# Kernel optimization log

Hardware: AMD Instinct MI355X
Metric: run time of the kernel (lower is better)

## Reference

```python
import jax, jax.numpy as jnp
import numpy as np

NEG_SLOPE = 0.1
BN_EPS = 1e-5

def leaky(x):
    return jnp.where(x >= 0, x, NEG_SLOPE * x)

def batchnorm(x, gamma, beta):
    # BatchNorm1d in training mode: biased batch stats over rows
    mu = jnp.mean(x, axis=0)
    var = jnp.var(x, axis=0)
    return gamma * (x - mu) * jax.lax.rsqrt(var + BN_EPS) + beta

def scatter_mean(x, idx, num_segments):
    s = jax.ops.segment_sum(x, idx, num_segments=num_segments)
    c = jax.ops.segment_sum(jnp.ones((x.shape[0], 1), x.dtype), idx, num_segments=num_segments)
    return s / jnp.maximum(c, 1.0)

def setup_inputs() -> dict:
    key = jax.random.key(0)
    ks = jax.random.split(key, 24)
    N, NF, MD, MO = 100000, 400000, 25000, 25000
    Cin, Cout = 64, 128
    Ch = Cout // 2
    def lin(k, fi, fo):
        kw, kb = jax.random.split(k)
        bound = 1.0 / np.sqrt(fi)
        W = jax.random.uniform(kw, (fi, fo), jnp.float32, -bound, bound)
        b = jax.random.uniform(kb, (fo,), jnp.float32, -bound, bound)
        return W, b
    W_in, b_in = lin(ks[0], Cin, Cout)
    W1, b1 = lin(ks[1], Cin, Ch)
    W2, b2 = lin(ks[2], Ch, Ch)
    W3, b3 = lin(ks[3], Ch, Cout)
    W4, b4 = lin(ks[4], 2 * Cout, Cout)
    W5, b5 = lin(ks[5], Cout, Cout)
    return {
        'features': jax.random.normal(ks[6], (N, Cin), jnp.float32),
        'inv': jax.random.randint(ks[7], (N,), 0, MD),
        'coors_inv_cur': jax.random.randint(ks[8], (NF,), 0, N),
        'coors_inv_next': jax.random.randint(ks[9], (NF,), 0, MO),
        'n_down': MD, 'n_out': MO,
        'W_in': W_in, 'b_in': b_in,
        'W1': W1, 'b1': b1, 'g1': jnp.ones((Ch,)), 'be1': jnp.zeros((Ch,)),
        'W2': W2, 'b2': b2, 'g2': jnp.ones((Ch,)), 'be2': jnp.zeros((Ch,)),
        'W3': W3, 'b3': b3,
        'W4': W4, 'b4': b4, 'W5': W5, 'b5': b5,
    }

def reference(features, inv, coors_inv_cur, coors_inv_next, n_down, n_out,
              W_in, b_in, W1, b1, g1, be1, W2, b2, g2, be2, W3, b3,
              W4, b4, W5, b5):
    # downsample: voxel-mean pooling of current-scale features  [MD, Cin]
    down = scatter_mean(features, inv, n_down)
    # identity branch  [N, Cout]
    identity = leaky(features @ W_in + b_in)
    # PPmodel MLP on pooled voxels
    h = batchnorm(leaky(down @ W1 + b1), g1, be1)
    h = batchnorm(leaky(h @ W2 + b2), g2, be2)
    h = leaky(h @ W3 + b3)                      # [MD, Cout]
    out = jnp.concatenate([identity, h[inv]], axis=1)   # [N, 2*Cout]
    g = out[coors_inv_cur]                      # gather to full points [NF, 2*Cout]
    g = leaky(g @ W4 + b4) @ W5 + b5            # layer_out [NF, Cout]
    v_feat = scatter_mean(g, coors_inv_next, n_out)      # [MO, Cout]
    return v_feat
```

## Files before the change

### kernel.cpp

```cpp
#include <hip/hip_runtime.h>
#include <hip/hip_bf16.h>

#define NEG_SLOPE 0.1f
#define BN_EPS 1e-5f
#define MDV 25000
#define CAPI 64
#define CAPD 32

typedef __bf16 bf16_t;
typedef bf16_t bf16x8 __attribute__((ext_vector_type(8)));
typedef float f32x4 __attribute__((ext_vector_type(4)));

__device__ __forceinline__ float leaky(float x) { return x >= 0.0f ? x : NEG_SLOPE * x; }

__global__ void k_setup(int4* __restrict__ zp, int n4, int nz,
                        const float* __restrict__ W4, const float* __restrict__ W5,
                        const float* __restrict__ Win, const float* __restrict__ W1,
                        bf16_t* __restrict__ P1, bf16_t* __restrict__ P2,
                        bf16_t* __restrict__ P0, bf16_t* __restrict__ P4) {
    if ((int)blockIdx.x < nz) {
        int i = blockIdx.x * 256 + threadIdx.x;
        if (i < n4) zp[i] = make_int4(0, 0, 0, 0);
        return;
    }
    int tid = (blockIdx.x - nz) * 256 + threadIdx.x;
    if (tid < 7168) {
        const float* W; bf16_t* P; int t;
        if (tid < 4096)      { W = W4;  P = P1; t = tid; }
        else if (tid < 6144) { W = W5;  P = P2; t = tid - 4096; }
        else                 { W = Win; P = P0; t = tid - 6144; }
        int l = t & 63;
        int sn = t >> 6;
        int col = (sn & 7) * 16 + (l & 15);
        int k0 = (sn >> 3) * 32 + (l >> 4) * 8;
        bf16_t* dst = P + (size_t)t * 8;
#pragma unroll
        for (int j = 0; j < 8; j++) dst[j] = (bf16_t)W[(size_t)(k0 + j) * 128 + col];
    } else if (tid < 7680) {
        int t = tid - 7168;
        int l = t & 63;
        int sn = t >> 6;
        int col = (sn & 3) * 16 + (l & 15);
        int k0 = (sn >> 2) * 32 + (l >> 4) * 8;
        bf16_t* dst = P4 + (size_t)t * 8;
#pragma unroll
        for (int j = 0; j < 8; j++) dst[j] = (bf16_t)W1[(size_t)(k0 + j) * 64 + col];
    }
}

__device__ __forceinline__ void two_gemm_tile(
        const float* __restrict__ in, const bf16_t* __restrict__ Pa,
        const float* __restrict__ ba, const bf16_t* __restrict__ Pb,
        const float* __restrict__ bb, bf16_t* __restrict__ out,
        int M, int base, bf16_t* A, bf16_t* C) {
    int tid = threadIdx.x;
    int valid = M - base; if (valid > 64) valid = 64;

    {
        int r = tid >> 2, q = tid & 3;
        float4 v[4];
        if (r < valid) {
            const float4* src = reinterpret_cast<const float4*>(in + (size_t)(base + r) * 64 + q * 16);
#pragma unroll
            for (int i = 0; i < 4; i++) v[i] = src[i];
        } else {
#pragma unroll
            for (int i = 0; i < 4; i++) v[i] = make_float4(0.f, 0.f, 0.f, 0.f);
        }
        bf16x8 h0, h1;
#pragma unroll
        for (int i = 0; i < 2; i++) {
            h0[i * 4 + 0] = (bf16_t)v[i].x; h0[i * 4 + 1] = (bf16_t)v[i].y;
            h0[i * 4 + 2] = (bf16_t)v[i].z; h0[i * 4 + 3] = (bf16_t)v[i].w;
            h1[i * 4 + 0] = (bf16_t)v[2 + i].x; h1[i * 4 + 1] = (bf16_t)v[2 + i].y;
            h1[i * 4 + 2] = (bf16_t)v[2 + i].z; h1[i * 4 + 3] = (bf16_t)v[2 + i].w;
        }
        int xa = (r & 7) << 3;
        *reinterpret_cast<bf16x8*>(&A[r * 64 + ((q * 16) ^ xa)]) = h0;
        *reinterpret_cast<bf16x8*>(&A[r * 64 + ((q * 16 + 8) ^ xa)]) = h1;
    }
    __syncthreads();

    int w = tid >> 6, l = tid & 63;
    int lg = l >> 4, lr = l & 15;
    int xr = (lr & 7) << 3;

    f32x4 acc[4][2];
#pragma unroll
    for (int t = 0; t < 2; t++) {
        float bv = ba[w * 32 + t * 16 + lr];
#pragma unroll
        for (int m = 0; m < 4; m++) acc[m][t] = (f32x4){bv, bv, bv, bv};
    }
#pragma unroll
    for (int s = 0; s < 2; s++) {
        bf16x8 a[4];
#pragma unroll
        for (int m = 0; m < 4; m++)
            a[m] = *reinterpret_cast<const bf16x8*>(&A[(m * 16 + lr) * 64 + (((s * 4 + lg) * 8) ^ xr)]);
#pragma unroll
        for (int t = 0; t < 2; t++) {
            bf16x8 b = *reinterpret_cast<const bf16x8*>(Pa + ((size_t)(s * 8 + w * 2 + t) * 64 + l) * 8);
#pragma unroll
            for (int m = 0; m < 4; m++)
                acc[m][t] = __builtin_amdgcn_mfma_f32_16x16x32_bf16(a[m], b, acc[m][t], 0, 0, 0);
        }
    }
#pragma unroll
    for (int m = 0; m < 4; m++)
#pragma unroll
        for (int t = 0; t < 2; t++)
#pragma unroll
            for (int rr = 0; rr < 4; rr++) {
                int row = m * 16 + lg * 4 + rr;
                int col = w * 32 + t * 16 + lr;
                C[row * 128 + (col ^ ((row & 7) << 3))] = (bf16_t)leaky(acc[m][t][rr]);
            }
    __syncthreads();

    f32x4 acc2[4][2];
#pragma unroll
    for (int t = 0; t < 2; t++) {
        float bv = bb ? bb[w * 32 + t * 16 + lr] : 0.0f;
#pragma unroll
        for (int m = 0; m < 4; m++) acc2[m][t] = (f32x4){bv, bv, bv, bv};
    }
#pragma unroll
    for (int s = 0; s < 4; s++) {
        bf16x8 a[4];
#pragma unroll
        for (int m = 0; m < 4; m++)
            a[m] = *reinterpret_cast<const bf16x8*>(&C[(m * 16 + lr) * 128 + ((s * 32 + lg * 8) ^ xr)]);
#pragma unroll
        for (int t = 0; t < 2; t++) {
            bf16x8 b = *reinterpret_cast<const bf16x8*>(Pb + ((size_t)(s * 8 + w * 2 + t) * 64 + l) * 8);
#pragma unroll
            for (int m = 0; m < 4; m++)
                acc2[m][t] = __builtin_amdgcn_mfma_f32_16x16x32_bf16(a[m], b, acc2[m][t], 0, 0, 0);
        }
    }
    __syncthreads();

#pragma unroll
    for (int m = 0; m < 4; m++)
#pragma unroll
        for (int t = 0; t < 2; t++)
#pragma unroll
            for (int rr = 0; rr < 4; rr++) {
                int row = m * 16 + lg * 4 + rr;
                int col = w * 32 + t * 16 + lr;
                C[row * 128 + (col ^ ((row & 7) << 3))] = (bf16_t)acc2[m][t][rr];
            }
    __syncthreads();
#pragma unroll
    for (int i = 0; i < 4; i++) {
        int u = tid + i * 256;
        int row = u >> 4, seg = u & 15;
        if (row < valid) {
            bf16x8 val = *reinterpret_cast<const bf16x8*>(&C[row * 128 + ((seg * 8) ^ ((row & 7) << 3))]);
            *reinterpret_cast<bf16x8*>(&out[(size_t)(base + row) * 128 + seg * 8]) = val;
        }
    }
}

__global__ __launch_bounds__(256) void k_build_z1(
        const int* __restrict__ inv, int* __restrict__ cntD, int* __restrict__ csrD,
        const int* __restrict__ nxt, const int* __restrict__ cur,
        int* __restrict__ cntI, int2* __restrict__ csrAB, int N, int NF, int nh,
        const float* __restrict__ feat, const bf16_t* __restrict__ P0,
        const float* __restrict__ bin, const bf16_t* __restrict__ P1,
        const float* __restrict__ b4, bf16_t* __restrict__ z1) {
    __shared__ bf16_t A[64 * 64];
    __shared__ bf16_t C[64 * 128];
    if ((int)blockIdx.x < nh) {
        int f = blockIdx.x * 256 + threadIdx.x;
        if (f < N) {
            int v = inv[f];
            int pos = atomicAdd(&cntD[v], 1);
            if (pos < CAPD) csrD[(size_t)v * CAPD + pos] = f;
        }
        if (f < NF) {
            int v = nxt[f];
            int pos = atomicAdd(&cntI[v], 1);
            int c = cur[f];
            if (pos < CAPI) csrAB[(size_t)v * CAPI + pos] = make_int2(c, inv[c]);
        }
        return;
    }
    two_gemm_tile(feat, P0, bin, P1, b4, z1, N, (blockIdx.x - nh) * 64, A, C);
}

__global__ __launch_bounds__(256) void k_downsum(
        const float* __restrict__ feat, const int* __restrict__ csrD,
        const int* __restrict__ cntD, float* __restrict__ dsum, int MD) {
    int w = threadIdx.x >> 6, l = threadIdx.x & 63;
    int q = l >> 4, sub = l & 15;
    int vox = blockIdx.x * 4 + w;
    if (vox >= MD) return;
    int cnt = cntD[vox];
    int cc = cnt < CAPD ? cnt : CAPD;
    size_t start = (size_t)vox * CAPD;
    float4 s = make_float4(0.f, 0.f, 0.f, 0.f);
    int p = 0;
    for (; p + 8 <= cc; p += 8) {
        int r0 = csrD[start + p + q];
        int r1 = csrD[start + p + 4 + q];
        float4 v0 = *reinterpret_cast<const float4*>(&feat[(size_t)r0 * 64 + sub * 4]);
        float4 v1 = *reinterpret_cast<const float4*>(&feat[(size_t)r1 * 64 + sub * 4]);
        s.x += v0.x + v1.x; s.y += v0.y + v1.y;
        s.z += v0.z + v1.z; s.w += v0.w + v1.w;
    }
    for (; p + 4 <= cc; p += 4) {
        int r0 = csrD[start + p + q];
        float4 v0 = *reinterpret_cast<const float4*>(&feat[(size_t)r0 * 64 + sub * 4]);
        s.x += v0.x; s.y += v0.y; s.z += v0.z; s.w += v0.w;
    }
    if (q < cc - p) {
        int r0 = csrD[start + p + q];
        float4 v0 = *reinterpret_cast<const float4*>(&feat[(size_t)r0 * 64 + sub * 4]);
        s.x += v0.x; s.y += v0.y; s.z += v0.z; s.w += v0.w;
    }
    s.x += __shfl_xor(s.x, 16); s.x += __shfl_xor(s.x, 32);
    s.y += __shfl_xor(s.y, 16); s.y += __shfl_xor(s.y, 32);
    s.z += __shfl_xor(s.z, 16); s.z += __shfl_xor(s.z, 32);
    s.w += __shfl_xor(s.w, 16); s.w += __shfl_xor(s.w, 32);
    if (q == 0) {
        float sc = (cc > 0) ? (1.0f / (float)cc) : 0.0f;
        float4 mv = make_float4(s.x * sc, s.y * sc, s.z * sc, s.w * sc);
        *reinterpret_cast<float4*>(&dsum[(size_t)vox * 64 + sub * 4]) = mv;
    }
}

__global__ __launch_bounds__(256) void k_mfma_bn(
        const float* __restrict__ in, const bf16_t* __restrict__ Pb,
        const float* __restrict__ bias, float* __restrict__ out,
        float* __restrict__ ssum, float* __restrict__ ssq, int M) {
    __shared__ bf16_t A[64 * 64];
    int tid = threadIdx.x;
    int base = blockIdx.x * 64;
    int valid = M - base; if (valid > 64) valid = 64;

    {
        int r = tid >> 2, q = tid & 3;
        float4 v[4];
        if (r < valid) {
            const float4* src = reinterpret_cast<const float4*>(in + (size_t)(base + r) * 64 + q * 16);
#pragma unroll
            for (int i = 0; i < 4; i++) v[i] = src[i];
        } else {
#pragma unroll
            for (int i = 0; i < 4; i++) v[i] = make_float4(0.f, 0.f, 0.f, 0.f);
        }
        bf16x8 h0, h1;
#pragma unroll
        for (int i = 0; i < 2; i++) {
            h0[i * 4 + 0] = (bf16_t)v[i].x; h0[i * 4 + 1] = (bf16_t)v[i].y;
            h0[i * 4 + 2] = (bf16_t)v[i].z; h0[i * 4 + 3] = (bf16_t)v[i].w;
            h1[i * 4 + 0] = (bf16_t)v[2 + i].x; h1[i * 4 + 1] = (bf16_t)v[2 + i].y;
            h1[i * 4 + 2] = (bf16_t)v[2 + i].z; h1[i * 4 + 3] = (bf16_t)v[2 + i].w;
        }
        int xa = (r & 7) << 3;
        *reinterpret_cast<bf16x8*>(&A[r * 64 + ((q * 16) ^ xa)]) = h0;
        *reinterpret_cast<bf16x8*>(&A[r * 64 + ((q * 16 + 8) ^ xa)]) = h1;
    }
    __syncthreads();

    int w = tid >> 6, l = tid & 63;
    int lg = l >> 4, lr = l & 15;
    int xr = (lr & 7) << 3;
    int col = w * 16 + lr;

    f32x4 acc[4];
    float bv = bias[col];
#pragma unroll
    for (int m = 0; m < 4; m++) acc[m] = (f32x4){bv, bv, bv, bv};
#pragma unroll
    for (int s = 0; s < 2; s++) {
        bf16x8 b = *reinterpret_cast<const bf16x8*>(Pb + ((size_t)((s * 4 + w) * 64 + l)) * 8);
#pragma unroll
        for (int m = 0; m < 4; m++) {
            bf16x8 a = *reinterpret_cast<const bf16x8*>(&A[(m * 16 + lr) * 64 + (((s * 4 + lg) * 8) ^ xr)]);
            acc[m] = __builtin_amdgcn_mfma_f32_16x16x32_bf16(a, b, acc[m], 0, 0, 0);
        }
    }

    float cs = 0.f, cq = 0.f;
#pragma unroll
    for (int m = 0; m < 4; m++) {
#pragma unroll
        for (int rr = 0; rr < 4; rr++) {
            int row = m * 16 + lg * 4 + rr;
            float val = leaky(acc[m][rr]);
            if (row < valid) {
                out[(size_t)(base + row) * 64 + col] = val;
                cs += val;
                cq += val * val;
            }
        }
    }
    cs += __shfl_xor(cs, 16); cs += __shfl_xor(cs, 32);
    cq += __shfl_xor(cq, 16); cq += __shfl_xor(cq, 32);
    if (lg == 0) {
        atomicAdd(&ssum[col], cs);
        atomicAdd(&ssq[col], cq);
    }
}

__global__ void k_fold(const float* __restrict__ ssum, const float* __restrict__ ssq,
                       const float* __restrict__ g, const float* __restrict__ be,
                       const float* __restrict__ W, const float* __restrict__ b,
                       bf16_t* __restrict__ Pp, float* __restrict__ bp, int M) {
    int j = threadIdx.x;
    if (j >= 64) return;
    float fM = (float)M;
    float accb = b[j];
    int n = j >> 4, jr = j & 15;
    for (int k = 0; k < 64; k++) {
        float mu = ssum[k] / fM;
        float var = ssq[k] / fM - mu * mu;
        float rstd = rsqrtf(var + BN_EPS);
        float ak = g[k] * rstd;
        float ck = be[k] - mu * ak;
        float w = W[k * 64 + j];
        accb = fmaf(ck, w, accb);
        int s = k >> 5, l = ((k >> 3) & 3) * 16 + jr, jj = k & 7;
        Pp[((size_t)((s * 4 + n) * 64 + l)) * 8 + jj] = (bf16_t)(ak * w);
    }
    bp[j] = accb;
}

__global__ void k_fold_packed(const float* __restrict__ ssum, const float* __restrict__ ssq,
                              const float* __restrict__ g, const float* __restrict__ be,
                              const float* __restrict__ W, const float* __restrict__ b,
                              bf16_t* __restrict__ P, float* __restrict__ bp, int M) {
    int j = threadIdx.x;
    if (j >= 128) return;
    float fM = (float)M;
    float accb = b[j];
    int n = j >> 4, jr = j & 15;
    for (int k = 0; k < 64; k++) {
        float mu = ssum[k] / fM;
        float var = ssq[k] / fM - mu * mu;
        float rstd = rsqrtf(var + BN_EPS);
        float ak = g[k] * rstd;
        float ck = be[k] - mu * ak;
        float w = W[k * 128 + j];
        accb = fmaf(ck, w, accb);
        int s = k >> 5, l = ((k >> 3) & 3) * 16 + jr, jj = k & 7;
        P[((size_t)((s * 8 + n) * 64 + l)) * 8 + jj] = (bf16_t)(ak * w);
    }
    bp[j] = accb;
}

__global__ __launch_bounds__(256) void k_two_gemm(
        const float* __restrict__ in, const bf16_t* __restrict__ Pa,
        const float* __restrict__ ba, const bf16_t* __restrict__ Pb,
        bf16_t* __restrict__ out, int M) {
    __shared__ bf16_t A[64 * 64];
    __shared__ bf16_t C[64 * 128];
    two_gemm_tile(in, Pa, ba, Pb, nullptr, out, M, blockIdx.x * 64, A, C);
}

__global__ __launch_bounds__(256) void k_gather_mean(
        const bf16_t* __restrict__ z1, const bf16_t* __restrict__ z2,
        const int2* __restrict__ csrAB, const int* __restrict__ cntI,
        bf16_t* __restrict__ meanB, int MO) {
    int w = threadIdx.x >> 6, l = threadIdx.x & 63;
    int q = l >> 4, sub = l & 15;
    int v = blockIdx.x * 4 + w;
    if (v >= MO) return;
    int cnt = cntI[v];
    int cc = cnt < CAPI ? cnt : CAPI;
    size_t start = (size_t)v * CAPI;
    float s[8] = {0.f, 0.f, 0.f, 0.f, 0.f, 0.f, 0.f, 0.f};
    int p = 0;
    for (; p + 16 <= cc; p += 16) {
        int2 e0 = csrAB[start + p + q];
        int2 e1 = csrAB[start + p + 4 + q];
        int2 e2 = csrAB[start + p + 8 + q];
        int2 e3 = csrAB[start + p + 12 + q];
        bf16x8 a0 = *reinterpret_cast<const bf16x8*>(&z1[(size_t)e0.x * 128 + sub * 8]);
        bf16x8 b0 = *reinterpret_cast<const bf16x8*>(&z2[(size_t)e0.y * 128 + sub * 8]);
        bf16x8 a1 = *reinterpret_cast<const bf16x8*>(&z1[(size_t)e1.x * 128 + sub * 8]);
        bf16x8 b1 = *reinterpret_cast<const bf16x8*>(&z2[(size_t)e1.y * 128 + sub * 8]);
        bf16x8 a2 = *reinterpret_cast<const bf16x8*>(&z1[(size_t)e2.x * 128 + sub * 8]);
        bf16x8 b2 = *reinterpret_cast<const bf16x8*>(&z2[(size_t)e2.y * 128 + sub * 8]);
        bf16x8 a3 = *reinterpret_cast<const bf16x8*>(&z1[(size_t)e3.x * 128 + sub * 8]);
        bf16x8 b3 = *reinterpret_cast<const bf16x8*>(&z2[(size_t)e3.y * 128 + sub * 8]);
#pragma unroll
        for (int j = 0; j < 8; j++) {
            s[j] += leaky((float)a0[j] + (float)b0[j]);
            s[j] += leaky((float)a1[j] + (float)b1[j]);
            s[j] += leaky((float)a2[j] + (float)b2[j]);
            s[j] += leaky((float)a3[j] + (float)b3[j]);
        }
    }
    for (; p + 8 <= cc; p += 8) {
        int2 e0 = csrAB[start + p + q];
        int2 e1 = csrAB[start + p + 4 + q];
        bf16x8 a0 = *reinterpret_cast<const bf16x8*>(&z1[(size_t)e0.x * 128 + sub * 8]);
        bf16x8 b0 = *reinterpret_cast<const bf16x8*>(&z2[(size_t)e0.y * 128 + sub * 8]);
        bf16x8 a1 = *reinterpret_cast<const bf16x8*>(&z1[(size_t)e1.x * 128 + sub * 8]);
        bf16x8 b1 = *reinterpret_cast<const bf16x8*>(&z2[(size_t)e1.y * 128 + sub * 8]);
#pragma unroll
        for (int j = 0; j < 8; j++) {
            s[j] += leaky((float)a0[j] + (float)b0[j]);
            s[j] += leaky((float)a1[j] + (float)b1[j]);
        }
    }
    for (; p + 4 <= cc; p += 4) {
        int2 e = csrAB[start + p + q];
        bf16x8 a = *reinterpret_cast<const bf16x8*>(&z1[(size_t)e.x * 128 + sub * 8]);
        bf16x8 b = *reinterpret_cast<const bf16x8*>(&z2[(size_t)e.y * 128 + sub * 8]);
#pragma unroll
        for (int j = 0; j < 8; j++) s[j] += leaky((float)a[j] + (float)b[j]);
    }
    if (q < cc - p) {
        int2 e = csrAB[start + p + q];
        bf16x8 a = *reinterpret_cast<const bf16x8*>(&z1[(size_t)e.x * 128 + sub * 8]);
        bf16x8 b = *reinterpret_cast<const bf16x8*>(&z2[(size_t)e.y * 128 + sub * 8]);
#pragma unroll
        for (int j = 0; j < 8; j++) s[j] += leaky((float)a[j] + (float)b[j]);
    }
    float sc = (cc > 0) ? (1.0f / (float)cc) : 0.0f;
#pragma unroll
    for (int j = 0; j < 8; j++) {
        s[j] += __shfl_xor(s[j], 16);
        s[j] += __shfl_xor(s[j], 32);
    }
    if (q == 0) {
        bf16x8 mv;
#pragma unroll
        for (int j = 0; j < 8; j++) mv[j] = (bf16_t)(s[j] * sc);
        *reinterpret_cast<bf16x8*>(&meanB[(size_t)v * 128 + sub * 8]) = mv;
    }
}

__global__ __launch_bounds__(256) void k_vox2(
        const bf16_t* __restrict__ meanB, const int* __restrict__ cntI,
        const bf16_t* __restrict__ P2, const float* __restrict__ b5,
        float* __restrict__ outp, int MO) {
    int tid = threadIdx.x;
    int base = blockIdx.x * 64;
    int w = tid >> 6, l = tid & 63;
    int lg = l >> 4, lr = l & 15;
    f32x4 acc[4][2];
#pragma unroll
    for (int t = 0; t < 2; t++) {
        float bv = b5[w * 32 + t * 16 + lr];
#pragma unroll
        for (int m = 0; m < 4; m++) acc[m][t] = (f32x4){bv, bv, bv, bv};
    }
#pragma unroll
    for (int s = 0; s < 4; s++) {
        bf16x8 a[4];
#pragma unroll
        for (int m = 0; m < 4; m++) {
            int row = base + m * 16 + lr;
            a[m] = *reinterpret_cast<const bf16x8*>(&meanB[(size_t)row * 128 + (s * 4 + lg) * 8]);
        }
#pragma unroll
        for (int t = 0; t < 2; t++) {
            bf16x8 b = *reinterpret_cast<const bf16x8*>(P2 + ((size_t)(s * 8 + w * 2 + t) * 64 + l) * 8);
#pragma unroll
            for (int m = 0; m < 4; m++)
                acc[m][t] = __builtin_amdgcn_mfma_f32_16x16x32_bf16(a[m], b, acc[m][t], 0, 0, 0);
        }
    }
#pragma unroll
    for (int m = 0; m < 4; m++)
#pragma unroll
        for (int t = 0; t < 2; t++)
#pragma unroll
            for (int rr = 0; rr < 4; rr++) {
                int row = base + m * 16 + lg * 4 + rr;
                if (row < MO) {
                    float val = (cntI[row] > 0) ? acc[m][t][rr] : 0.0f;
                    outp[(size_t)row * 128 + w * 32 + t * 16 + lr] = val;
                }
            }
}

extern "C" void kernel_launch(void* const* d_in, const int* in_sizes, int n_in,
                              void* d_out, int out_size, void* d_ws, size_t ws_size,
                              hipStream_t stream) {
    const float* feat = (const float*)d_in[0];
    const int*   inv  = (const int*)d_in[1];
    const int*   cur  = (const int*)d_in[2];
    const int*   nxt  = (const int*)d_in[3];
    const float* W_in = (const float*)d_in[6];
    const float* b_in = (const float*)d_in[7];
    const float* W1   = (const float*)d_in[8];
    const float* b1   = (const float*)d_in[9];
    const float* g1   = (const float*)d_in[10];
    const float* be1  = (const float*)d_in[11];
    const float* W2   = (const float*)d_in[12];
    const float* b2   = (const float*)d_in[13];
    const float* g2   = (const float*)d_in[14];
    const float* be2  = (const float*)d_in[15];
    const float* W3   = (const float*)d_in[16];
    const float* b3   = (const float*)d_in[17];
    const float* W4   = (const float*)d_in[18];
    const float* b4   = (const float*)d_in[19];
    const float* W5   = (const float*)d_in[20];
    const float* b5   = (const float*)d_in[21];

    const int N  = in_sizes[0] / 64;
    const int NF = in_sizes[2];
    const int MO = out_size / 128;
    const int MD = MDV;

    float* ws = (float*)d_ws;
    size_t off = 0;
    float* ssum1 = ws + off; off += 64;
    float* ssq1  = ws + off; off += 64;
    float* ssum2 = ws + off; off += 64;
    float* ssq2  = ws + off; off += 64;
    int* cntD    = (int*)(ws + off); off += (size_t)MD;
    int* cntI    = (int*)(ws + off); off += (size_t)MO;
    off = (off + 3) & ~(size_t)3;
    size_t zeroElems = off;
    float* dsum = ws + off; off += (size_t)MD * 64;
    float* t1   = ws + off; off += (size_t)MD * 64;
    float* t2   = ws + off; off += (size_t)MD * 64;
    float* bp2  = ws + off; off += 64;
    float* bp3  = ws + off; off += 128;
    int* csrD   = (int*)(ws + off); off += (size_t)MD * CAPD;
    off = (off + 1) & ~(size_t)1;
    int2* csrAB = (int2*)(ws + off); off += (size_t)MO * CAPI * 2;
    bf16_t* bws = (bf16_t*)(ws + off);
    size_t boff = 0;
    bf16_t* z1    = bws + boff; boff += (size_t)N * 128;
    bf16_t* z2    = bws + boff; boff += (size_t)MD * 128;
    bf16_t* meanB = bws + boff; boff += (size_t)MO * 128 + 4096;
    bf16_t* P0    = bws + boff; boff += 8192;
    bf16_t* P1    = bws + boff; boff += 32768;
    bf16_t* P2    = bws + boff; boff += 16384;
    bf16_t* P3    = bws + boff; boff += 8192;
    bf16_t* P4    = bws + boff; boff += 4096;
    bf16_t* P5    = bws + boff; boff += 4096;
    (void)ws_size; (void)n_in;

    int n4 = (int)(zeroElems >> 2);
    int nz = (n4 + 255) / 256;
    k_setup<<<nz + 30, 256, 0, stream>>>((int4*)d_ws, n4, nz, W4, W5, W_in, W1, P1, P2, P0, P4);

    int gmax = (NF > N ? NF : N);
    int nh = (gmax + 255) / 256;
    int nt2 = (N + 63) / 64;
    k_build_z1<<<nh + nt2, 256, 0, stream>>>(inv, cntD, csrD, nxt, cur, cntI, csrAB,
                                             N, NF, nh, feat, P0, b_in, P1, b4, z1);

    k_downsum<<<(MD + 3) / 4, 256, 0, stream>>>(feat, csrD, cntD, dsum, MD);
    k_mfma_bn<<<(MD + 63) / 64, 256, 0, stream>>>(dsum, P4, b1, t1, ssum1, ssq1, MD);
    k_fold<<<1, 64, 0, stream>>>(ssum1, ssq1, g1, be1, W2, b2, P5, bp2, MD);
    k_mfma_bn<<<(MD + 63) / 64, 256, 0, stream>>>(t1, P5, bp2, t2, ssum2, ssq2, MD);
    k_fold_packed<<<1, 128, 0, stream>>>(ssum2, ssq2, g2, be2, W3, b3, P3, bp3, MD);

    k_two_gemm<<<(MD + 63) / 64, 256, 0, stream>>>(t2, P3, bp3, P1 + 16384, z2, MD);

    k_gather_mean<<<(MO + 3) / 4, 256, 0, stream>>>(z1, z2, csrAB, cntI, meanB, MO);
    k_vox2<<<(MO + 63) / 64, 256, 0, stream>>>(meanB, cntI, P2, b5, (float*)d_out, MO);
}
```

Before: 165.6 us.

## Split CSR-AB construction into four chunks fused into small MD kernels

Moves the scatter-style build of the NF-point CSR (atomic counters plus int2 index writes) out of the first big kernel and spreads it in four chunks across the downsum, two BN-GEMM, and z2 GEMM launches as extra blocks. Those MD-sized kernels are small and leave the GPU underused, so the atomic index build can fill idle compute units instead of lengthening the first kernel. The risk is contention between the atomic traffic and the GEMM blocks, plus extra parameters and branch overhead in each kernel.

```diff
diff --git a/kernel.cpp b/kernel.cpp
--- a/kernel.cpp
+++ b/kernel.cpp
@@ -12,6 +12,15 @@
 typedef float f32x4 __attribute__((ext_vector_type(4)));
 
 __device__ __forceinline__ float leaky(float x) { return x >= 0.0f ? x : NEG_SLOPE * x; }
+
+__device__ __forceinline__ void build_ab(const int* __restrict__ nxt, const int* __restrict__ cur,
+                                         const int* __restrict__ inv, int* __restrict__ cntI,
+                                         int2* __restrict__ csrAB, int f) {
+    int v = nxt[f];
+    int pos = atomicAdd(&cntI[v], 1);
+    int c = cur[f];
+    if (pos < CAPI) csrAB[(size_t)v * CAPI + pos] = make_int2(c, inv[c]);
+}
 
 __global__ void k_setup(int4* __restrict__ zp, int n4, int nz,
                         const float* __restrict__ W4, const float* __restrict__ W5,
@@ -163,36 +172,37 @@
     }
 }
 
-__global__ __launch_bounds__(256) void k_build_z1(
+__global__ __launch_bounds__(256) void k_buildD_z1(
         const int* __restrict__ inv, int* __restrict__ cntD, int* __restrict__ csrD,
-        const int* __restrict__ nxt, const int* __restrict__ cur,
-        int* __restrict__ cntI, int2* __restrict__ csrAB, int N, int NF, int nh,
+        int N, int nhD,
         const float* __restrict__ feat, const bf16_t* __restrict__ P0,
         const float* __restrict__ bin, const bf16_t* __restrict__ P1,
         const float* __restrict__ b4, bf16_t* __restrict__ z1) {
     __shared__ bf16_t A[64 * 64];
     __shared__ bf16_t C[64 * 128];
-    if ((int)blockIdx.x < nh) {
+    if ((int)blockIdx.x < nhD) {
         int f = blockIdx.x * 256 + threadIdx.x;
         if (f < N) {
             int v = inv[f];
             int pos = atomicAdd(&cntD[v], 1);
             if (pos < CAPD) csrD[(size_t)v * CAPD + pos] = f;
         }
-        if (f < NF) {
-            int v = nxt[f];
-            int pos = atomicAdd(&cntI[v], 1);
-            int c = cur[f];
-            if (pos < CAPI) csrAB[(size_t)v * CAPI + pos] = make_int2(c, inv[c]);
-        }
         return;
     }
-    two_gemm_tile(feat, P0, bin, P1, b4, z1, N, (blockIdx.x - nh) * 64, A, C);
+    two_gemm_tile(feat, P0, bin, P1, b4, z1, N, (blockIdx.x - nhD) * 64, A, C);
 }
 
 __global__ __launch_bounds__(256) void k_downsum(
         const float* __restrict__ feat, const int* __restrict__ csrD,
-        const int* __restrict__ cntD, float* __restrict__ dsum, int MD) {
+        const int* __restrict__ cntD, float* __restrict__ dsum, int MD, int nmain,
+        const int* __restrict__ nxt, const int* __restrict__ cur,
+        const int* __restrict__ inv, int* __restrict__ cntI,
+        int2* __restrict__ csrAB, int f0, int f1) {
+    if ((int)blockIdx.x >= nmain) {
+        int f = f0 + (blockIdx.x - nmain) * 256 + threadIdx.x;
+        if (f < f1) build_ab(nxt, cur, inv, cntI, csrAB, f);
+        return;
+    }
     int w = threadIdx.x >> 6, l = threadIdx.x & 63;
     int q = l >> 4, sub = l & 15;
     int vox = blockIdx.x * 4 + w;
@@ -234,8 +244,16 @@
 __global__ __launch_bounds__(256) void k_mfma_bn(
         const float* __restrict__ in, const bf16_t* __restrict__ Pb,
         const float* __restrict__ bias, float* __restrict__ out,
-        float* __restrict__ ssum, float* __restrict__ ssq, int M) {
+        float* __restrict__ ssum, float* __restrict__ ssq, int M, int nmain,
+        const int* __restrict__ nxt, const int* __restrict__ cur,
+        const int* __restrict__ inv, int* __restrict__ cntI,
+        int2* __restrict__ csrAB, int f0, int f1) {
     __shared__ bf16_t A[64 * 64];
+    if ((int)blockIdx.x >= nmain) {
+        int f = f0 + (blockIdx.x - nmain) * 256 + threadIdx.x;
+        if (f < f1) build_ab(nxt, cur, inv, cntI, csrAB, f);
+        return;
+    }
     int tid = threadIdx.x;
     int base = blockIdx.x * 64;
     int valid = M - base; if (valid > 64) valid = 64;
@@ -355,9 +373,17 @@
 __global__ __launch_bounds__(256) void k_two_gemm(
         const float* __restrict__ in, const bf16_t* __restrict__ Pa,
         const float* __restrict__ ba, const bf16_t* __restrict__ Pb,
-        bf16_t* __restrict__ out, int M) {
+        bf16_t* __restrict__ out, int M, int nmain,
+        const int* __restrict__ nxt, const int* __restrict__ cur,
+        const int* __restrict__ inv, int* __restrict__ cntI,
+        int2* __restrict__ csrAB, int f0, int f1) {
     __shared__ bf16_t A[64 * 64];
     __shared__ bf16_t C[64 * 128];
+    if ((int)blockIdx.x >= nmain) {
+        int f = f0 + (blockIdx.x - nmain) * 256 + threadIdx.x;
+        if (f < f1) build_ab(nxt, cur, inv, cntI, csrAB, f);
+        return;
+    }
     two_gemm_tile(in, Pa, ba, Pb, nullptr, out, M, blockIdx.x * 64, A, C);
 }
 
@@ -545,19 +571,31 @@
     int nz = (n4 + 255) / 256;
     k_setup<<<nz + 30, 256, 0, stream>>>((int4*)d_ws, n4, nz, W4, W5, W_in, W1, P1, P2, P0, P4);
 
-    int gmax = (NF > N ? NF : N);
-    int nh = (gmax + 255) / 256;
+    int nhD = (N + 255) / 256;
     int nt2 = (N + 63) / 64;
-    k_build_z1<<<nh + nt2, 256, 0, stream>>>(inv, cntD, csrD, nxt, cur, cntI, csrAB,
-                                             N, NF, nh, feat, P0, b_in, P1, b4, z1);
-
-    k_downsum<<<(MD + 3) / 4, 256, 0, stream>>>(feat, csrD, cntD, dsum, MD);
-    k_mfma_bn<<<(MD + 63) / 64, 256, 0, stream>>>(dsum, P4, b1, t1, ssum1, ssq1, MD);
+    k_buildD_z1<<<nhD + nt2, 256, 0, stream>>>(inv, cntD, csrD, N, nhD,
+                                               feat, P0, b_in, P1, b4, z1);
+
+    int chunk = (NF + 3) / 4;
+    int f0a = 0,        f1a = chunk;
+    int f0b = chunk,    f1b = 2 * chunk;
+    int f0c = 2 * chunk, f1c = 3 * chunk;
+    int f0d = 3 * chunk, f1d = NF;
+    int cb = (chunk + 255) / 256;
+
+    int nds = (MD + 3) / 4;
+    k_downsum<<<nds + cb, 256, 0, stream>>>(feat, csrD, cntD, dsum, MD, nds,
+                                            nxt, cur, inv, cntI, csrAB, f0a, f1a);
+    int nmb = (MD + 63) / 64;
+    k_mfma_bn<<<nmb + cb, 256, 0, stream>>>(dsum, P4, b1, t1, ssum1, ssq1, MD, nmb,
+                                            nxt, cur, inv, cntI, csrAB, f0b, f1b);
     k_fold<<<1, 64, 0, stream>>>(ssum1, ssq1, g1, be1, W2, b2, P5, bp2, MD);
-    k_mfma_bn<<<(MD + 63) / 64, 256, 0, stream>>>(t1, P5, bp2, t2, ssum2, ssq2, MD);
+    k_mfma_bn<<<nmb + cb, 256, 0, stream>>>(t1, P5, bp2, t2, ssum2, ssq2, MD, nmb,
+                                            nxt, cur, inv, cntI, csrAB, f0c, f1c);
     k_fold_packed<<<1, 128, 0, stream>>>(ssum2, ssq2, g2, be2, W3, b3, P3, bp3, MD);
 
-    k_two_gemm<<<(MD + 63) / 64, 256, 0, stream>>>(t2, P3, bp3, P1 + 16384, z2, MD);
+    k_two_gemm<<<nmb + cb, 256, 0, stream>>>(t2, P3, bp3, P1 + 16384, z2, MD, nmb,
+                                             nxt, cur, inv, cntI, csrAB, f0d, f1d);
 
     k_gather_mean<<<(MO + 3) / 4, 256, 0, stream>>>(z1, z2, csrAB, cntI, meanB, MO);
     k_vox2<<<(MO + 63) / 64, 256, 0, stream>>>(meanB, cntI, P2, b5, (float*)d_out, MO);
```

Measured after the change: 164.5 us. No clear change (-0.7%).
